# Optimization experiments

Hardware: AMD Instinct MI355X
Metric: run time of the kernel (lower is better)

The kernel has to match this reference:

```python
import jax, jax.numpy as jnp
import numpy as np

D = 1024
H = 16
K = D // H
B = 2
S = 2048

def setup_inputs() -> dict:
    key = jax.random.key(0)
    k1, k2, k3, k4, k5 = jax.random.split(key, 5)
    x = jax.random.normal(k1, (B, S, D), dtype=jnp.float32)
    # nn.Linear(d, 3d): weight [3d, d], bias [3d]
    Wqkv = jax.random.normal(k2, (3 * D, D), dtype=jnp.float32) / np.sqrt(D)
    bqkv = jax.random.normal(k3, (3 * D,), dtype=jnp.float32) * 0.01
    Wproj = jax.random.normal(k4, (D, D), dtype=jnp.float32) / np.sqrt(D)
    bproj = jax.random.normal(k5, (D,), dtype=jnp.float32) * 0.01
    return {"x": x, "Wqkv": Wqkv, "bqkv": bqkv, "Wproj": Wproj, "bproj": bproj}

def reference(x, Wqkv, bqkv, Wproj, bproj):
    Bsz, Slen, d = x.shape
    # fused QKV projection: [B,S,3d] -> [B,S,3,H,K] -> (3, B, H, S, K)
    qkv = (jnp.einsum('bsd,ed->bse', x, Wqkv) + bqkv).reshape(Bsz, Slen, 3, H, K)
    q, k, v = jnp.moveaxis(qkv, 2, 0).transpose(0, 1, 3, 2, 4)
    scale = 1.0 / jnp.sqrt(jnp.asarray(K, dtype=x.dtype))
    scores = jnp.einsum('bhqk,bhmk->bhqm', q, k) * scale  # [B,H,S,S]
    a = jax.nn.softmax(scores, axis=-1)
    # dropout is identity in eval mode
    o = jnp.einsum('bhqm,bhmk->bhqk', a, v)  # [B,H,S,K]
    o = o.transpose(0, 2, 1, 3).reshape(Bsz, Slen, d)
    return jnp.einsum('bsd,ed->bse', o, Wproj) + bproj
```

## Files before the change

### kernel.cpp

```cpp
#include <hip/hip_runtime.h>
#include <cstdint>

typedef unsigned short ushort_t;
typedef short short8 __attribute__((ext_vector_type(8)));
typedef float f32x4 __attribute__((ext_vector_type(4)));
typedef float float4v __attribute__((ext_vector_type(4)));
typedef unsigned int uint2v __attribute__((ext_vector_type(2)));

#define DDIM 1024
#define HH 16
#define HEADK 64
#define BB 2
#define SS 2048

#if __has_builtin(__builtin_amdgcn_exp2f)
#define EXP2F(x) __builtin_amdgcn_exp2f(x)
#else
#define EXP2F(x) exp2f(x)
#endif

__device__ __forceinline__ ushort_t f2bf(float f) {
  union { float f; uint32_t u; } c; c.f = f;
  uint32_t u = c.u;
  u += 0x7fffu + ((u >> 16) & 1u);
  return (ushort_t)(u >> 16);
}

__device__ __forceinline__ uint32_t pkbf_trunc(float a, float b) {
  union { float f; uint32_t u; } ca, cb;
  ca.f = a; cb.f = b;
  return __builtin_amdgcn_perm(cb.u, ca.u, 0x07060302);
}

__device__ __forceinline__ uint32_t pkbf_rne(float a, float b) {
  return (uint32_t)f2bf(a) | ((uint32_t)f2bf(b) << 16);
}

__device__ __forceinline__ void glds16(const ushort_t* gp, ushort_t* lp) {
  __builtin_amdgcn_global_load_lds(
      (const __attribute__((address_space(1))) uint32_t*)gp,
      (__attribute__((address_space(3))) uint32_t*)lp, 16, 0, 0);
}

__global__ void cvt3_kernel(const float* __restrict__ s0, ushort_t* __restrict__ d0, int n0,
                            const float* __restrict__ s1, ushort_t* __restrict__ d1, int n1,
                            const float* __restrict__ s2, ushort_t* __restrict__ d2, int n2) {
  int i = blockIdx.x * blockDim.x + threadIdx.x;
  const float* src; ushort_t* dst; int k;
  if (i < n0) { src = s0; dst = d0; k = i; }
  else if (i < n0 + n1) { src = s1; dst = d1; k = i - n0; }
  else if (i < n0 + n1 + n2) { src = s2; dst = d2; k = i - n0 - n1; }
  else return;
  float4v v = ((const float4v*)src)[k];
  uint2v o; o[0] = pkbf_rne(v[0], v[1]); o[1] = pkbf_rne(v[2], v[3]);
  ((uint2v*)dst)[k] = o;
}

template <int MODE>
__global__ __launch_bounds__(256) void gemm_nt(
    const ushort_t* __restrict__ A, const ushort_t* __restrict__ Bm,
    const float* __restrict__ bias, float* __restrict__ Cout,
    ushort_t* __restrict__ Cbf, int M, int N, int Kd) {
  __shared__ ushort_t As[128 * 64];
  __shared__ ushort_t Bs[128 * 64];
  const int tid = threadIdx.x;
  const int wv = tid >> 6, lane = tid & 63;
  const int l15 = lane & 15, quad = lane >> 4;
  const int wm = wv >> 1, wn = wv & 1;
  const int tm0 = blockIdx.y * 128, tn0 = blockIdx.x * 128;

  f32x4 acc[4][4];
#pragma unroll
  for (int i = 0; i < 4; ++i)
#pragma unroll
    for (int j = 0; j < 4; ++j) acc[i][j] = (f32x4){0.f, 0.f, 0.f, 0.f};

  const int lrow = lane >> 3;
  const int gcb = (lane & 7) ^ lrow;

  for (int k0 = 0; k0 < Kd; k0 += 64) {
#pragma unroll
    for (int c = 0; c < 4; ++c) {
      int seg = wv * 4 + c;
      glds16(A + (size_t)(tm0 + seg * 8 + lrow) * Kd + k0 + gcb * 8,
             As + seg * 512);
    }
#pragma unroll
    for (int c = 0; c < 4; ++c) {
      int seg = wv * 4 + c;
      glds16(Bm + (size_t)(tn0 + seg * 8 + lrow) * Kd + k0 + gcb * 8,
             Bs + seg * 512);
    }
    __syncthreads();
#pragma unroll
    for (int kk = 0; kk < 64; kk += 32) {
      short8 af[4], bfr[4];
#pragma unroll
      for (int i = 0; i < 4; ++i) {
        int r = wm * 64 + i * 16 + l15;
        int cb = (kk >> 3) + quad;
        af[i] = *(const short8*)(As + r * 64 + ((cb ^ (l15 & 7)) << 3));
      }
#pragma unroll
      for (int j = 0; j < 4; ++j) {
        int r = wn * 64 + j * 16 + l15;
        int cb = (kk >> 3) + quad;
        bfr[j] = *(const short8*)(Bs + r * 64 + ((cb ^ (l15 & 7)) << 3));
      }
#pragma unroll
      for (int i = 0; i < 4; ++i)
#pragma unroll
        for (int j = 0; j < 4; ++j)
          acc[i][j] = __builtin_amdgcn_mfma_f32_16x16x32_bf16(
              af[i], bfr[j], acc[i][j], 0, 0, 0);
    }
    __syncthreads();
  }

#pragma unroll
  for (int j = 0; j < 4; ++j) {
    int col = tn0 + wn * 64 + j * 16 + l15;
    float bv = bias[col];
#pragma unroll
    for (int i = 0; i < 4; ++i) {
      int row0 = tm0 + wm * 64 + i * 16 + quad * 4;
#pragma unroll
      for (int r = 0; r < 4; ++r) {
        float v = acc[i][j][r] + bv;
        int row = row0 + r;
        if (MODE == 0) {
          int t = col >> 10, hh = (col >> 6) & 15, kk2 = col & 63;
          int b = row >> 11, s = row & 2047;
          float vv = (t == 0) ? v * 0.18033688f : v;
          size_t base = (((size_t)t * BB + b) * HH + hh) * ((size_t)SS * HEADK);
          size_t idx = (t == 2) ? base + (size_t)kk2 * SS + s
                                : base + (size_t)s * HEADK + kk2;
          Cbf[idx] = f2bf(vv);
        } else {
          Cout[(size_t)row * N + col] = v;
        }
      }
    }
  }
}

__global__ __launch_bounds__(128, 2) void attn_kernel(
    const ushort_t* __restrict__ qkv, ushort_t* __restrict__ ob) {
  __shared__ ushort_t Kt[2][64 * 64];
  __shared__ ushort_t Vt[2][64 * 64];
  __shared__ ushort_t Pw[2][32 * 64];

  const int qt = blockIdx.x, h = blockIdx.y, b = blockIdx.z;
  const int tid = threadIdx.x;
  const int wv = tid >> 6, lane = tid & 63;
  const int l15 = lane & 15, quad = lane >> 4;

  const size_t hstride = (size_t)SS * HEADK;
  const ushort_t* Qg = qkv + ((size_t)(0 * BB + b) * HH + h) * hstride;
  const ushort_t* Kg = qkv + ((size_t)(1 * BB + b) * HH + h) * hstride;
  const ushort_t* Vg = qkv + ((size_t)(2 * BB + b) * HH + h) * hstride;

  short8 qf[2][2];
#pragma unroll
  for (int mi = 0; mi < 2; ++mi)
#pragma unroll
    for (int kc = 0; kc < 2; ++kc)
      qf[mi][kc] = *(const short8*)(
          Qg + (size_t)(qt * 64 + wv * 32 + mi * 16 + l15) * 64 + kc * 32 +
          quad * 8);

  const short ONE = (short)0x3F80;
  short8 ones = {ONE, ONE, ONE, ONE, ONE, ONE, ONE, ONE};

  f32x4 oat[2][4];
  f32x4 loa[2];
#pragma unroll
  for (int mi = 0; mi < 2; ++mi) {
    loa[mi] = (f32x4){0.f, 0.f, 0.f, 0.f};
#pragma unroll
    for (int c = 0; c < 4; ++c) oat[mi][c] = (f32x4){0.f, 0.f, 0.f, 0.f};
  }

  const int lrow = lane >> 3, gcb = (lane & 7) ^ lrow;

  auto stage = [&](int jj, int db) {
#pragma unroll
    for (int c = 0; c < 4; ++c) {
      int seg = wv * 4 + c;
      glds16(Kg + (size_t)(jj * 64 + seg * 8 + lrow) * 64 + gcb * 8,
             &Kt[db][seg * 512]);
    }
#pragma unroll
    for (int c = 0; c < 4; ++c) {
      int seg = wv * 4 + c;
      glds16(Vg + (size_t)(seg * 8 + lrow) * SS + jj * 64 + gcb * 8,
             &Vt[db][seg * 512]);
    }
  };

  stage(0, 0);

  for (int j = 0; j < 32; ++j) {
    const int db = j & 1;
    __syncthreads();
    if (j + 1 < 32) stage(j + 1, db ^ 1);

    f32x4 st[2][4];
#pragma unroll
    for (int cf = 0; cf < 4; ++cf) {
      int n = cf * 16 + l15;
      short8 kf0 = *(const short8*)(&Kt[db][n * 64 + ((quad ^ (n & 7)) << 3)]);
      short8 kf1 =
          *(const short8*)(&Kt[db][n * 64 + (((quad + 4) ^ (n & 7)) << 3)]);
#pragma unroll
      for (int mi = 0; mi < 2; ++mi) {
        f32x4 z = (f32x4){0.f, 0.f, 0.f, 0.f};
        z = __builtin_amdgcn_mfma_f32_16x16x32_bf16(kf0, qf[mi][0], z, 0, 0, 0);
        z = __builtin_amdgcn_mfma_f32_16x16x32_bf16(kf1, qf[mi][1], z, 0, 0, 0);
        st[mi][cf] = z;
      }
    }

#pragma unroll
    for (int mi = 0; mi < 2; ++mi)
#pragma unroll
      for (int cf = 0; cf < 4; ++cf) {
        float e0 = EXP2F(st[mi][cf][0]);
        float e1 = EXP2F(st[mi][cf][1]);
        float e2 = EXP2F(st[mi][cf][2]);
        float e3 = EXP2F(st[mi][cf][3]);
        uint2v dw;
        dw[0] = pkbf_trunc(e0, e1);
        dw[1] = pkbf_trunc(e2, e3);
        int row = mi * 16 + l15;
        int bb = 2 * cf + (quad >> 1);
        *(uint2v*)(&Pw[wv][row * 64 + ((bb ^ (l15 & 7)) << 3) +
                           (quad & 1) * 4]) = dw;
      }

    short8 pa[2][2];
#pragma unroll
    for (int mi = 0; mi < 2; ++mi)
#pragma unroll
      for (int kc = 0; kc < 2; ++kc)
        pa[mi][kc] = *(const short8*)(&Pw[wv][(mi * 16 + l15) * 64 +
                                              (((kc * 4 + quad) ^ (l15 & 7))
                                               << 3)]);

#pragma unroll
    for (int cf = 0; cf < 4; ++cf) {
      int f = cf * 16 + l15;
      short8 vb0 = *(const short8*)(&Vt[db][f * 64 + ((quad ^ (f & 7)) << 3)]);
      short8 vb1 =
          *(const short8*)(&Vt[db][f * 64 + (((quad + 4) ^ (f & 7)) << 3)]);
#pragma unroll
      for (int mi = 0; mi < 2; ++mi) {
        oat[mi][cf] = __builtin_amdgcn_mfma_f32_16x16x32_bf16(
            vb0, pa[mi][0], oat[mi][cf], 0, 0, 0);
        oat[mi][cf] = __builtin_amdgcn_mfma_f32_16x16x32_bf16(
            vb1, pa[mi][1], oat[mi][cf], 0, 0, 0);
      }
    }
#pragma unroll
    for (int mi = 0; mi < 2; ++mi) {
      loa[mi] = __builtin_amdgcn_mfma_f32_16x16x32_bf16(ones, pa[mi][0],
                                                        loa[mi], 0, 0, 0);
      loa[mi] = __builtin_amdgcn_mfma_f32_16x16x32_bf16(ones, pa[mi][1],
                                                        loa[mi], 0, 0, 0);
    }
  }

#pragma unroll
  for (int mi = 0; mi < 2; ++mi) {
    float inv = 1.0f / loa[mi][0];
#pragma unroll
    for (int cf = 0; cf < 4; ++cf) {
      uint2v dw;
      dw[0] = pkbf_rne(oat[mi][cf][0] * inv, oat[mi][cf][1] * inv);
      dw[1] = pkbf_rne(oat[mi][cf][2] * inv, oat[mi][cf][3] * inv);
      int row = mi * 16 + l15;
      int bb = 2 * cf + (quad >> 1);
      *(uint2v*)(&Pw[wv][row * 64 + ((bb ^ (l15 & 7)) << 3) + (quad & 1) * 4]) =
          dw;
    }
  }
  const int rr = lane >> 1, half = lane & 1;
#pragma unroll
  for (int c = 0; c < 4; ++c) {
    short8 ov = *(const short8*)(&Pw[wv][rr * 64 +
                                         (((half * 4 + c) ^ (rr & 7)) << 3)]);
    int row = qt * 64 + wv * 32 + rr;
    *(short8*)(&ob[(size_t)(b * SS + row) * DDIM + h * 64 + half * 32 +
                   c * 8]) = ov;
  }
}

extern "C" void kernel_launch(void* const* d_in, const int* in_sizes, int n_in,
                              void* d_out, int out_size, void* d_ws,
                              size_t ws_size, hipStream_t stream) {
  const float* x = (const float*)d_in[0];
  const float* Wqkv = (const float*)d_in[1];
  const float* bqkv = (const float*)d_in[2];
  const float* Wproj = (const float*)d_in[3];
  const float* bproj = (const float*)d_in[4];
  float* out = (float*)d_out;

  ushort_t* xb = (ushort_t*)d_ws;
  ushort_t* wqb = xb + (size_t)4096 * 1024;
  ushort_t* wpb = wqb + (size_t)3072 * 1024;
  ushort_t* qkvb = wpb + (size_t)1024 * 1024;
  ushort_t* obuf = qkvb + (size_t)3 * BB * HH * SS * HEADK;

  const int n0 = 4096 * 1024 / 4, n1 = 3072 * 1024 / 4, n2 = 1024 * 1024 / 4;
  cvt3_kernel<<<(n0 + n1 + n2 + 255) / 256, 256, 0, stream>>>(
      x, xb, n0, Wqkv, wqb, n1, Wproj, wpb, n2);
  gemm_nt<0><<<dim3(3072 / 128, 4096 / 128), 256, 0, stream>>>(
      xb, wqb, bqkv, nullptr, qkvb, 4096, 3072, 1024);
  attn_kernel<<<dim3(SS / 64, HH, BB), 128, 0, stream>>>(qkvb, obuf);
  gemm_nt<1><<<dim3(1024 / 128, 4096 / 128), 256, 0, stream>>>(
      obuf, wpb, bproj, out, nullptr, 4096, 1024, 1024);
}
```

Measured before the change: 201.4 us.

## Load K/V fragments directly from global into registers, 4-wave blocks

Attention blocks grow to 256 threads covering 128 query rows and are indexed through a flattened grid that groups (head,batch) pairs. The shared-memory K/V double buffering with async global-to-LDS copies and per-iteration barriers is removed. Each wave now loads its own K and V MFMA fragments straight from global memory into registers, prefetching the next tile during the current compute. This drops LDS traffic and the __syncthreads stalls, but every wave redundantly fetches K/V from global/L2 and register pressure rises.

After: 265.1 us. 1.32x slower.

```diff
diff --git a/kernel.cpp b/kernel.cpp
--- a/kernel.cpp
+++ b/kernel.cpp
@@ -144,13 +144,13 @@
   }
 }
 
-__global__ __launch_bounds__(128, 2) void attn_kernel(
+__global__ __launch_bounds__(256, 2) void attn_kernel(
     const ushort_t* __restrict__ qkv, ushort_t* __restrict__ ob) {
-  __shared__ ushort_t Kt[2][64 * 64];
-  __shared__ ushort_t Vt[2][64 * 64];
-  __shared__ ushort_t Pw[2][32 * 64];
-
-  const int qt = blockIdx.x, h = blockIdx.y, b = blockIdx.z;
+  __shared__ ushort_t Pw[4][32 * 64];
+
+  const int bid = blockIdx.x;
+  const int p = bid & 31, qt = bid >> 5;
+  const int h = p >> 1, b = p & 1;
   const int tid = threadIdx.x;
   const int wv = tid >> 6, lane = tid & 63;
   const int l15 = lane & 15, quad = lane >> 4;
@@ -166,7 +166,7 @@
 #pragma unroll
     for (int kc = 0; kc < 2; ++kc)
       qf[mi][kc] = *(const short8*)(
-          Qg + (size_t)(qt * 64 + wv * 32 + mi * 16 + l15) * 64 + kc * 32 +
+          Qg + (size_t)(qt * 128 + wv * 32 + mi * 16 + l15) * 64 + kc * 32 +
           quad * 8);
 
   const short ONE = (short)0x3F80;
@@ -181,45 +181,36 @@
     for (int c = 0; c < 4; ++c) oat[mi][c] = (f32x4){0.f, 0.f, 0.f, 0.f};
   }
 
-  const int lrow = lane >> 3, gcb = (lane & 7) ^ lrow;
-
-  auto stage = [&](int jj, int db) {
-#pragma unroll
-    for (int c = 0; c < 4; ++c) {
-      int seg = wv * 4 + c;
-      glds16(Kg + (size_t)(jj * 64 + seg * 8 + lrow) * 64 + gcb * 8,
-             &Kt[db][seg * 512]);
-    }
-#pragma unroll
-    for (int c = 0; c < 4; ++c) {
-      int seg = wv * 4 + c;
-      glds16(Vg + (size_t)(seg * 8 + lrow) * SS + jj * 64 + gcb * 8,
-             &Vt[db][seg * 512]);
-    }
-  };
-
-  stage(0, 0);
+  short8 kf[4][2], vf[4][2];
+#pragma unroll
+  for (int cf = 0; cf < 4; ++cf)
+#pragma unroll
+    for (int kc = 0; kc < 2; ++kc) {
+      kf[cf][kc] = *(const short8*)(
+          Kg + (size_t)(cf * 16 + l15) * 64 + kc * 32 + quad * 8);
+      vf[cf][kc] = *(const short8*)(
+          Vg + (size_t)(cf * 16 + l15) * SS + kc * 32 + quad * 8);
+    }
 
   for (int j = 0; j < 32; ++j) {
-    const int db = j & 1;
-    __syncthreads();
-    if (j + 1 < 32) stage(j + 1, db ^ 1);
-
     f32x4 st[2][4];
 #pragma unroll
-    for (int cf = 0; cf < 4; ++cf) {
-      int n = cf * 16 + l15;
-      short8 kf0 = *(const short8*)(&Kt[db][n * 64 + ((quad ^ (n & 7)) << 3)]);
-      short8 kf1 =
-          *(const short8*)(&Kt[db][n * 64 + (((quad + 4) ^ (n & 7)) << 3)]);
+    for (int cf = 0; cf < 4; ++cf)
 #pragma unroll
       for (int mi = 0; mi < 2; ++mi) {
         f32x4 z = (f32x4){0.f, 0.f, 0.f, 0.f};
-        z = __builtin_amdgcn_mfma_f32_16x16x32_bf16(kf0, qf[mi][0], z, 0, 0, 0);
-        z = __builtin_amdgcn_mfma_f32_16x16x32_bf16(kf1, qf[mi][1], z, 0, 0, 0);
+        z = __builtin_amdgcn_mfma_f32_16x16x32_bf16(kf[cf][0], qf[mi][0], z, 0, 0, 0);
+        z = __builtin_amdgcn_mfma_f32_16x16x32_bf16(kf[cf][1], qf[mi][1], z, 0, 0, 0);
         st[mi][cf] = z;
       }
-    }
+
+    const int jn = (j + 1) & 31;
+#pragma unroll
+    for (int cf = 0; cf < 4; ++cf)
+#pragma unroll
+      for (int kc = 0; kc < 2; ++kc)
+        kf[cf][kc] = *(const short8*)(
+            Kg + (size_t)(jn * 64 + cf * 16 + l15) * 64 + kc * 32 + quad * 8);
 
 #pragma unroll
     for (int mi = 0; mi < 2; ++mi)
@@ -248,19 +239,14 @@
                                                << 3)]);
 
 #pragma unroll
-    for (int cf = 0; cf < 4; ++cf) {
-      int f = cf * 16 + l15;
-      short8 vb0 = *(const short8*)(&Vt[db][f * 64 + ((quad ^ (f & 7)) << 3)]);
-      short8 vb1 =
-          *(const short8*)(&Vt[db][f * 64 + (((quad + 4) ^ (f & 7)) << 3)]);
+    for (int cf = 0; cf < 4; ++cf)
 #pragma unroll
       for (int mi = 0; mi < 2; ++mi) {
         oat[mi][cf] = __builtin_amdgcn_mfma_f32_16x16x32_bf16(
-            vb0, pa[mi][0], oat[mi][cf], 0, 0, 0);
+            vf[cf][0], pa[mi][0], oat[mi][cf], 0, 0, 0);
         oat[mi][cf] = __builtin_amdgcn_mfma_f32_16x16x32_bf16(
-            vb1, pa[mi][1], oat[mi][cf], 0, 0, 0);
-      }
-    }
+            vf[cf][1], pa[mi][1], oat[mi][cf], 0, 0, 0);
+      }
 #pragma unroll
     for (int mi = 0; mi < 2; ++mi) {
       loa[mi] = __builtin_amdgcn_mfma_f32_16x16x32_bf16(ones, pa[mi][0],
@@ -268,6 +254,13 @@
       loa[mi] = __builtin_amdgcn_mfma_f32_16x16x32_bf16(ones, pa[mi][1],
                                                         loa[mi], 0, 0, 0);
     }
+
+#pragma unroll
+    for (int cf = 0; cf < 4; ++cf)
+#pragma unroll
+      for (int kc = 0; kc < 2; ++kc)
+        vf[cf][kc] = *(const short8*)(
+            Vg + (size_t)(cf * 16 + l15) * SS + jn * 64 + kc * 32 + quad * 8);
   }
 
 #pragma unroll
@@ -289,7 +282,7 @@
   for (int c = 0; c < 4; ++c) {
     short8 ov = *(const short8*)(&Pw[wv][rr * 64 +
                                          (((half * 4 + c) ^ (rr & 7)) << 3)]);
-    int row = qt * 64 + wv * 32 + rr;
+    int row = qt * 128 + wv * 32 + rr;
     *(short8*)(&ob[(size_t)(b * SS + row) * DDIM + h * 64 + half * 32 +
                    c * 8]) = ov;
   }
@@ -316,7 +309,7 @@
       x, xb, n0, Wqkv, wqb, n1, Wproj, wpb, n2);
   gemm_nt<0><<<dim3(3072 / 128, 4096 / 128), 256, 0, stream>>>(
       xb, wqb, bqkv, nullptr, qkvb, 4096, 3072, 1024);
-  attn_kernel<<<dim3(SS / 64, HH, BB), 128, 0, stream>>>(qkvb, obuf);
+  attn_kernel<<<dim3(512), 256, 0, stream>>>(qkvb, obuf);
   gemm_nt<1><<<dim3(1024 / 128, 4096 / 128), 256, 0, stream>>>(
       obuf, wpb, bproj, out, nullptr, 4096, 1024, 1024);
 }
```

## Stage transposed V epilogue through LDS and shrink output-projection GEMM tile

Applied to the files above, without the earlier changes.

The QKV GEMM epilogue now branches per tile on Q/K/V. For the V section, the transposed output is staged through swizzled shared memory so it can be written to global memory as 16-byte coalesced stores, replacing scattered 2-byte strided stores. The output-projection GEMM is also templated to use a 64-row M tile, which doubles its block count to 512 and improves occupancy across CUs. The costs are extra LDS traffic and barriers in the V epilogue, and less per-block reuse in the smaller projection tile.

Result: faster. 194.6 us (-3.4%).

```diff
diff --git a/kernel.cpp b/kernel.cpp
--- a/kernel.cpp
+++ b/kernel.cpp
@@ -56,32 +56,35 @@
   ((uint2v*)dst)[k] = o;
 }
 
-template <int MODE>
+template <int MODE, int TM>
 __global__ __launch_bounds__(256) void gemm_nt(
     const ushort_t* __restrict__ A, const ushort_t* __restrict__ Bm,
     const float* __restrict__ bias, float* __restrict__ Cout,
     ushort_t* __restrict__ Cbf, int M, int N, int Kd) {
-  __shared__ ushort_t As[128 * 64];
-  __shared__ ushort_t Bs[128 * 64];
+  __shared__ ushort_t smem[128 * 64 * 2];
+  ushort_t* As = smem;
+  ushort_t* Bs = smem + TM * 64;
+  const int MI = TM / 32;
   const int tid = threadIdx.x;
   const int wv = tid >> 6, lane = tid & 63;
   const int l15 = lane & 15, quad = lane >> 4;
   const int wm = wv >> 1, wn = wv & 1;
-  const int tm0 = blockIdx.y * 128, tn0 = blockIdx.x * 128;
-
-  f32x4 acc[4][4];
-#pragma unroll
-  for (int i = 0; i < 4; ++i)
+  const int tm0 = blockIdx.y * TM, tn0 = blockIdx.x * 128;
+
+  f32x4 acc[MI][4];
+#pragma unroll
+  for (int i = 0; i < MI; ++i)
 #pragma unroll
     for (int j = 0; j < 4; ++j) acc[i][j] = (f32x4){0.f, 0.f, 0.f, 0.f};
 
   const int lrow = lane >> 3;
   const int gcb = (lane & 7) ^ lrow;
+  const int ACI = TM / 32;
 
   for (int k0 = 0; k0 < Kd; k0 += 64) {
 #pragma unroll
-    for (int c = 0; c < 4; ++c) {
-      int seg = wv * 4 + c;
+    for (int c = 0; c < ACI; ++c) {
+      int seg = wv * ACI + c;
       glds16(A + (size_t)(tm0 + seg * 8 + lrow) * Kd + k0 + gcb * 8,
              As + seg * 512);
     }
@@ -94,10 +97,10 @@
     __syncthreads();
 #pragma unroll
     for (int kk = 0; kk < 64; kk += 32) {
-      short8 af[4], bfr[4];
-#pragma unroll
-      for (int i = 0; i < 4; ++i) {
-        int r = wm * 64 + i * 16 + l15;
+      short8 af[MI], bfr[4];
+#pragma unroll
+      for (int i = 0; i < MI; ++i) {
+        int r = wm * (TM / 2) + i * 16 + l15;
         int cb = (kk >> 3) + quad;
         af[i] = *(const short8*)(As + r * 64 + ((cb ^ (l15 & 7)) << 3));
       }
@@ -108,7 +111,7 @@
         bfr[j] = *(const short8*)(Bs + r * 64 + ((cb ^ (l15 & 7)) << 3));
       }
 #pragma unroll
-      for (int i = 0; i < 4; ++i)
+      for (int i = 0; i < MI; ++i)
 #pragma unroll
         for (int j = 0; j < 4; ++j)
           acc[i][j] = __builtin_amdgcn_mfma_f32_16x16x32_bf16(
@@ -117,28 +120,72 @@
     __syncthreads();
   }
 
-#pragma unroll
-  for (int j = 0; j < 4; ++j) {
-    int col = tn0 + wn * 64 + j * 16 + l15;
-    float bv = bias[col];
-#pragma unroll
-    for (int i = 0; i < 4; ++i) {
-      int row0 = tm0 + wm * 64 + i * 16 + quad * 4;
-#pragma unroll
-      for (int r = 0; r < 4; ++r) {
-        float v = acc[i][j][r] + bv;
-        int row = row0 + r;
-        if (MODE == 0) {
-          int t = col >> 10, hh = (col >> 6) & 15, kk2 = col & 63;
-          int b = row >> 11, s = row & 2047;
-          float vv = (t == 0) ? v * 0.18033688f : v;
-          size_t base = (((size_t)t * BB + b) * HH + hh) * ((size_t)SS * HEADK);
-          size_t idx = (t == 2) ? base + (size_t)kk2 * SS + s
-                                : base + (size_t)s * HEADK + kk2;
-          Cbf[idx] = f2bf(vv);
-        } else {
-          Cout[(size_t)row * N + col] = v;
+  if (MODE == 1) {
+#pragma unroll
+    for (int j = 0; j < 4; ++j) {
+      int col = tn0 + wn * 64 + j * 16 + l15;
+      float bv = bias[col];
+#pragma unroll
+      for (int i = 0; i < MI; ++i) {
+        int row0 = tm0 + wm * (TM / 2) + i * 16 + quad * 4;
+#pragma unroll
+        for (int r = 0; r < 4; ++r)
+          Cout[(size_t)(row0 + r) * N + col] = acc[i][j][r] + bv;
+      }
+    }
+  } else {
+    const int t = tn0 >> 10;
+    if (t < 2) {
+#pragma unroll
+      for (int j = 0; j < 4; ++j) {
+        int col = tn0 + wn * 64 + j * 16 + l15;
+        float bv = bias[col];
+        int hh = (col >> 6) & 15, kk2 = col & 63;
+#pragma unroll
+        for (int i = 0; i < MI; ++i) {
+          int row0 = tm0 + wm * (TM / 2) + i * 16 + quad * 4;
+#pragma unroll
+          for (int r = 0; r < 4; ++r) {
+            int row = row0 + r;
+            int b = row >> 11, s = row & 2047;
+            float v = acc[i][j][r] + bv;
+            if (t == 0) v *= 0.18033688f;
+            size_t base =
+                (((size_t)t * BB + b) * HH + hh) * ((size_t)SS * HEADK);
+            Cbf[base + (size_t)s * HEADK + kk2] = f2bf(v);
+          }
         }
+      }
+    } else {
+      __syncthreads();
+#pragma unroll
+      for (int j = 0; j < 4; ++j) {
+        int c = wn * 64 + j * 16 + l15;
+        float bv = bias[tn0 + c];
+#pragma unroll
+        for (int i = 0; i < MI; ++i) {
+          int row0 = wm * (TM / 2) + i * 16 + quad * 4;
+          uint2v dw;
+          dw[0] = pkbf_rne(acc[i][j][0] + bv, acc[i][j][1] + bv);
+          dw[1] = pkbf_rne(acc[i][j][2] + bv, acc[i][j][3] + bv);
+          int rb = row0 >> 3;
+          *(uint2v*)(&smem[c * 128 + (((rb ^ (c & 15)) << 3) | (row0 & 7))]) =
+              dw;
+        }
+      }
+      __syncthreads();
+      const int rb2 = lane & 15;
+      const int cg = lane >> 4;
+#pragma unroll
+      for (int it = 0; it < 8; ++it) {
+        int c = wv * 32 + it * 4 + cg;
+        short8 vv = *(const short8*)(&smem[c * 128 + ((rb2 ^ (c & 15)) << 3)]);
+        int gcol = tn0 + c;
+        int hh = (gcol >> 6) & 15, kk2 = gcol & 63;
+        int grow = tm0 + rb2 * 8;
+        int b = grow >> 11, s = grow & 2047;
+        size_t base = (((size_t)2 * BB + b) * HH + hh) * ((size_t)SS * HEADK);
+        *(short8*)(&Cbf[base + (size_t)kk2 * SS + s]) = vv;
       }
     }
   }
@@ -314,9 +361,9 @@
   const int n0 = 4096 * 1024 / 4, n1 = 3072 * 1024 / 4, n2 = 1024 * 1024 / 4;
   cvt3_kernel<<<(n0 + n1 + n2 + 255) / 256, 256, 0, stream>>>(
       x, xb, n0, Wqkv, wqb, n1, Wproj, wpb, n2);
-  gemm_nt<0><<<dim3(3072 / 128, 4096 / 128), 256, 0, stream>>>(
+  gemm_nt<0, 128><<<dim3(3072 / 128, 4096 / 128), 256, 0, stream>>>(
       xb, wqb, bqkv, nullptr, qkvb, 4096, 3072, 1024);
   attn_kernel<<<dim3(SS / 64, HH, BB), 128, 0, stream>>>(qkvb, obuf);
-  gemm_nt<1><<<dim3(1024 / 128, 4096 / 128), 256, 0, stream>>>(
+  gemm_nt<1, 64><<<dim3(1024 / 128, 4096 / 64), 256, 0, stream>>>(
       obuf, wpb, bproj, out, nullptr, 4096, 1024, 1024);
 }
```
